# Performance work log

Hardware: AMD Instinct MI355X
Metric: run time of the kernel (lower is better)

Reference implementation:

```python
import jax, jax.numpy as jnp
import numpy as np

N_CLASSES = 16
REG = 0.1


def setup_inputs() -> dict:
    key = jax.random.key(0)
    k1, k2, k3, k4 = jax.random.split(key, 4)
    N, M, d = 4096, 4096, 1024
    X = jax.random.normal(k1, (N, d), dtype=jnp.float32)
    y = jax.random.randint(k2, (N,), 0, N_CLASSES)
    Xq = jax.random.normal(k3, (M, d), dtype=jnp.float32)
    m = 0.01 * jax.random.normal(k4, (1, d), dtype=jnp.float32)
    kappa = jnp.asarray(0.1, dtype=jnp.float32)
    nu = jnp.asarray(float(d), dtype=jnp.float32)
    triu_diag = jnp.ones((d,), dtype=jnp.float32)
    triu_lower = jnp.eye(d, dtype=jnp.float32) + 0.01 * jax.random.normal(
        jax.random.fold_in(key, 7), (d, d), dtype=jnp.float32)
    return {"X": X, "y": y, "Xq": Xq, "m": m, "kappa": kappa, "nu": nu,
            "triu_diag": triu_diag, "triu_lower": triu_lower}


def reference(X, y, Xq, m, kappa, nu, triu_diag, triu_lower):
    d = X.shape[1]
    C = N_CLASSES
    # Cholesky-factor prior scale: diag(|triu_diag|) + strictly-lower part of triu_lower
    strict_lower = jnp.tril(jnp.ones((d, d), dtype=X.dtype), -1)
    L = jnp.diag(jnp.abs(triu_diag)) + triu_lower * strict_lower
    kap = jnp.abs(kappa) + 1e-6
    nu_ = jnp.maximum(nu, d - 1 + 1e-6)

    # --- fit (vectorized over classes) ---
    onehot = jax.nn.one_hot(y, C, dtype=X.dtype)          # [N, C]
    Nj = onehot.sum(axis=0)                               # [C]
    sums = onehot.T @ X                                   # [C, d] grouped sums
    means = sums / Nj[:, None]                            # [C, d]
    mu = (kap / (kap + Nj))[:, None] * m + (Nj / (kap + Nj))[:, None] * means  # [C, d]
    # grouped scatter: S[c] = X_c^T X_c, via class-weighted features
    Xw = X[:, None, :] * onehot[:, :, None]               # [N, C, d]
    S = jnp.einsum('ncd,ne->cde', Xw, X)                  # [C, d, d]
    base = L @ L.T + kap * (m.T @ m)                      # [d, d]
    sigma = (base[None] + S
             - (kap + Nj)[:, None, None] * jnp.einsum('cd,ce->cde', mu, mu))
    sigma = sigma / (nu_ + Nj + d + 2)[:, None, None]     # [C, d, d]
    eye = jnp.eye(d, dtype=X.dtype)
    sigma_inv = (1.0 - REG) * jnp.linalg.inv(sigma) + REG * eye[None]

    # --- predict: negative Mahalanobis quadratic form per (query, class) ---
    diff = Xq[:, None, :] - mu[None]                      # [M, C, d]
    logits = -jnp.einsum('mcd,cde,mce->mc', diff, sigma_inv, diff)  # [M, C]
    return logits
```

## Files before the change

### kernel.cpp

```cpp
#include <hip/hip_runtime.h>
#include <math.h>

#define DD 1024
#define NP 5120
#define PT_TILES 80
#define TS 65

typedef _Float16 half8 __attribute__((ext_vector_type(8)));
typedef _Float16 half4 __attribute__((ext_vector_type(4)));
typedef float floatx4 __attribute__((ext_vector_type(4)));
typedef short s16x8 __attribute__((ext_vector_type(8)));

#define OFF_XTH   ((size_t)0)
#define OFF_XTL   ((size_t)2621440)
#define OFF_BASE  ((size_t)5242880)
#define OFF_SIGMA ((size_t)6291456)
#define OFF_DINV  ((size_t)23068672)
#define OFF_SUMS  ((size_t)24117248)
#define OFF_MU    ((size_t)24133632)
#define OFF_U     ((size_t)24150016)
#define OFF_MU2   ((size_t)24166400)
#define OFF_XQ2   ((size_t)24166416)
#define OFF_XQMU  ((size_t)24170512)
#define OFF_KAPNU ((size_t)24236048)
#define OFF_CF    ((size_t)24236056)
#define OFF_BETA  ((size_t)24236072)
#define OFF_INVS  ((size_t)24236088)
#define OFF_INTS  ((size_t)24236104)

#define UT_CLS_STRIDE ((size_t)557056)

__device__ __forceinline__ void tri_decode(int b, int& ti, int& tj) {
  int t = 0;
  while ((t + 1) * (t + 2) / 2 <= b) t++;
  ti = t;
  tj = b - t * (t + 1) / 2;
}

__device__ __forceinline__ short f2bf(float f) {
  union { float f; unsigned u; } v; v.f = f;
  unsigned r = v.u + 0x7FFF + ((v.u >> 16) & 1);
  return (short)(r >> 16);
}
__device__ __forceinline__ float bf2f(short b) {
  union { unsigned u; float f; } v; v.u = ((unsigned)(unsigned short)b) << 16; return v.f;
}

__device__ __forceinline__ float reduce256(float v, float* scratch) {
  for (int o = 32; o > 0; o >>= 1) v += __shfl_down(v, o, 64);
  int lane = threadIdx.x & 63, w = threadIdx.x >> 6;
  __syncthreads();
  if (lane == 0) scratch[w] = v;
  __syncthreads();
  return scratch[0] + scratch[1] + scratch[2] + scratch[3];
}

__global__ void k_scalars(const int* y, const float* kappa, const float* nu,
                          float* kapnu, float* cf, float* beta, float* invs,
                          int* counts, int* offsets, int* cls_of_pt, int* order,
                          float* sums, float* uarr, float* dout) {
  __shared__ int h[16];
  __shared__ int cur[16];
  int t = threadIdx.x;
  if (t < 16) h[t] = 0;
  __syncthreads();
  for (int n = t; n < 4096; n += 256) atomicAdd(&h[y[n]], 1);
  __syncthreads();
  if (t == 0) {
    float kap = fabsf(kappa[0]) + 1e-6f;
    float nu_ = fmaxf(nu[0], 1024.0f - 1.0f + 1e-6f);
    kapnu[0] = kap; kapnu[1] = nu_;
    int off = 0, tile = 0;
    for (int c = 0; c < 16; c++) {
      counts[c] = h[c]; offsets[c] = off; cur[c] = off;
      cf[c] = (float)h[c];
      beta[c] = kap + (float)h[c];
      invs[c] = 1.0f / (nu_ + (float)h[c] + 1024.0f + 2.0f);
      int ntile = ((h[c] + 63) & ~63) >> 6;
      for (int q = 0; q < ntile && tile < PT_TILES; q++) cls_of_pt[tile++] = c;
      off += (h[c] + 63) & ~63;
    }
    while (tile < PT_TILES) cls_of_pt[tile++] = -1;
  }
  for (int i = t; i < NP; i += 256) order[i] = -1;
  for (int i = t; i < 16 * 1024; i += 256) { sums[i] = 0.f; uarr[i] = 0.f; }
  for (int i = t; i < 4096 * 16; i += 256) dout[i] = 0.f;
  __syncthreads();
  for (int n = t; n < 4096; n += 256) {
    int c = y[n];
    int p = atomicAdd(&cur[c], 1);
    order[p] = n;
  }
}

__global__ void k_gatherT(const float* X, const int* order, const int* cls_of_pt,
                          short* XTh, short* XTl, float* sums) {
  int pt = blockIdx.x, dt = blockIdx.y, t = threadIdx.x;
  __shared__ float T[64 * TS];
  __shared__ float CS[4 * 64];
  __shared__ int src[64];
  if (t < 64) src[t] = order[pt * 64 + t];
  __syncthreads();
  for (int i = 0; i < 4; i++) {
    int idx4 = i * 256 + t;
    int r = idx4 >> 4, c4 = (idx4 & 15) << 2;
    int s = src[r];
    float4 v = (s >= 0) ? *(const float4*)&X[(size_t)s * DD + dt * 64 + c4]
                        : make_float4(0.f, 0.f, 0.f, 0.f);
    T[r * TS + c4] = v.x; T[r * TS + c4 + 1] = v.y;
    T[r * TS + c4 + 2] = v.z; T[r * TS + c4 + 3] = v.w;
  }
  __syncthreads();
  for (int i = 0; i < 16; i++) {
    int lin = i * 256 + t;
    int d = lin >> 6, p = lin & 63;
    float v = T[p * TS + d];
    short hi = f2bf(v);
    float lov = v - bf2f(hi);
    size_t addr = (size_t)(dt * 64 + d) * NP + pt * 64 + p;
    XTh[addr] = hi;
    XTl[addr] = f2bf(lov);
  }
  int cls = cls_of_pt[pt];
  if (cls < 0) return;
  int g = t >> 6, d = t & 63;
  float s = 0.f;
  for (int p = g * 16; p < g * 16 + 16; p++) s += T[p * TS + d];
  CS[g * 64 + d] = s;
  __syncthreads();
  if (g == 0)
    atomicAdd(&sums[(size_t)cls * DD + dt * 64 + d],
              CS[d] + CS[64 + d] + CS[128 + d] + CS[192 + d]);
}

__global__ void k_mumu2(const float* sums, const float* m, const float* kapnu,
                        const float* cf, float* mu, float* mu2) {
  __shared__ float scratch[4];
  int c = blockIdx.x, t = threadIdx.x;
  float kap = kapnu[0];
  float denom = 1.0f / (kap + cf[c]);
  float s2 = 0.f;
  for (int j = t; j < DD; j += 256) {
    float v = (kap * m[j] + sums[(size_t)c * DD + j]) * denom;
    mu[(size_t)c * DD + j] = v;
    s2 += v * v;
  }
  float tot = reduce256(s2, scratch);
  if (t == 0) mu2[c] = tot;
}

__device__ __forceinline__ float lval(const float* td, const float* tl, int i, int j) {
  if (i == j) return fabsf(td[i]);
  if (i > j) return tl[(size_t)i * DD + j];
  return 0.f;
}

__global__ void k_base(const float* td, const float* tl, const float* m,
                       const float* kapnu, float* base) {
  int ti, tj; tri_decode(blockIdx.x, ti, tj);
  __shared__ float Ta[16][65], Tb[16][65];
  int t = threadIdx.x, tx = t & 15, ty = t >> 4;
  int r0 = ty * 4, c0 = tx * 4;
  float acc[4][4] = {};
  int kmax = (tj + 1) * 64;
  for (int kk = 0; kk < kmax; kk += 16) {
    __syncthreads();
    for (int idx = t; idx < 64 * 16; idx += 256) {
      int r = idx >> 4, p = idx & 15;
      Ta[p][r] = lval(td, tl, ti * 64 + r, kk + p);
      Tb[p][r] = lval(td, tl, tj * 64 + r, kk + p);
    }
    __syncthreads();
#pragma unroll
    for (int p = 0; p < 16; p++) {
      float av[4], bv[4];
#pragma unroll
      for (int a = 0; a < 4; a++) av[a] = Ta[p][r0 + a];
#pragma unroll
      for (int b = 0; b < 4; b++) bv[b] = Tb[p][c0 + b];
#pragma unroll
      for (int a = 0; a < 4; a++)
#pragma unroll
        for (int b = 0; b < 4; b++) acc[a][b] += av[a] * bv[b];
    }
  }
  float kap = kapnu[0];
#pragma unroll
  for (int a = 0; a < 4; a++)
#pragma unroll
    for (int b = 0; b < 4; b++) {
      int gi = ti * 64 + r0 + a, gj = tj * 64 + c0 + b;
      base[(size_t)gi * DD + gj] = acc[a][b] + kap * m[gi] * m[gj];
    }
}

__global__ __launch_bounds__(256) void k_syrk_mfma(const short* XTh, const short* XTl,
                                                   const float* base, const float* mu,
                                                   const float* beta, const float* invs,
                                                   const int* counts, const int* offsets,
                                                   float* sigma) {
  int bb = blockIdx.x;
  int cls = bb / 36, tr = bb % 36;
  int ti, tj; tri_decode(tr, ti, tj);
  int cnt = counts[cls], off = offsets[cls];
  float* Sg = sigma + ((size_t)cls << 20);
  const float* muc = mu + (size_t)cls * DD;
  __shared__ short Ah[128 * 40], Al[128 * 40], Bh[128 * 40], Bl[128 * 40];
  int t = threadIdx.x;
  int wave = t >> 6, lane = t & 63;
  int wr = wave >> 1, wc = wave & 1;
  int quad = lane >> 4, l15 = lane & 15;
  int i0 = ti * 128, j0 = tj * 128;
  bool same = (ti == tj);
  floatx4 acc[4][4];
#pragma unroll
  for (int a = 0; a < 4; a++)
#pragma unroll
    for (int b = 0; b < 4; b++) acc[a][b] = (floatx4){0.f, 0.f, 0.f, 0.f};
  for (int nn = 0; nn < cnt; nn += 32) {
    __syncthreads();
#pragma unroll
    for (int r = 0; r < 2; r++) {
      int lin = r * 256 + t;
      int row = lin >> 2, kg = (lin & 3) << 3;
      size_t sA = (size_t)(i0 + row) * NP + off + nn + kg;
      *(s16x8*)&Ah[row * 40 + kg] = *(const s16x8*)&XTh[sA];
      *(s16x8*)&Al[row * 40 + kg] = *(const s16x8*)&XTl[sA];
      if (!same) {
        size_t sB = (size_t)(j0 + row) * NP + off + nn + kg;
        *(s16x8*)&Bh[row * 40 + kg] = *(const s16x8*)&XTh[sB];
        *(s16x8*)&Bl[row * 40 + kg] = *(const s16x8*)&XTl[sB];
      }
    }
    __syncthreads();
    const short* PBh = same ? Ah : Bh;
    const short* PBl = same ? Al : Bl;
    s16x8 ah[4], al[4], bh[4], bl[4];
#pragma unroll
    for (int f = 0; f < 4; f++) {
      ah[f] = *(const s16x8*)&Ah[(wr * 64 + f * 16 + l15) * 40 + quad * 8];
      al[f] = *(const s16x8*)&Al[(wr * 64 + f * 16 + l15) * 40 + quad * 8];
      bh[f] = *(const s16x8*)&PBh[(wc * 64 + f * 16 + l15) * 40 + quad * 8];
      bl[f] = *(const s16x8*)&PBl[(wc * 64 + f * 16 + l15) * 40 + quad * 8];
    }
#pragma unroll
    for (int fi = 0; fi < 4; fi++)
#pragma unroll
      for (int fj = 0; fj < 4; fj++) {
        acc[fi][fj] = __builtin_amdgcn_mfma_f32_16x16x32_bf16(ah[fi], bh[fj], acc[fi][fj], 0, 0, 0);
        acc[fi][fj] = __builtin_amdgcn_mfma_f32_16x16x32_bf16(ah[fi], bl[fj], acc[fi][fj], 0, 0, 0);
        acc[fi][fj] = __builtin_amdgcn_mfma_f32_16x16x32_bf16(al[fi], bh[fj], acc[fi][fj], 0, 0, 0);
      }
  }
  float bet = beta[cls], isc = invs[cls];
#pragma unroll
  for (int fi = 0; fi < 4; fi++)
#pragma unroll
    for (int fj = 0; fj < 4; fj++)
#pragma unroll
      for (int reg = 0; reg < 4; reg++) {
        int gi = i0 + wr * 64 + fi * 16 + quad * 4 + reg;
        int gj = j0 + wc * 64 + fj * 16 + l15;
        float v = acc[fi][fj][reg] + base[(size_t)gi * DD + gj] - bet * muc[gi] * muc[gj];
        Sg[(size_t)gi * DD + gj] = v * isc;
      }
}

__device__ void chol_inv_reg(float areg[4][4], float* Dinv, int cls, int k, int t,
                             float* Asc, float* Wsc, float* Tsc) {
  __shared__ float colbuf[2][64];
  __shared__ float sdiag[64];
  int tx = t & 15, ty = t >> 4;
  int r0 = ty * 4, c0 = tx * 4;
  for (int j = 0; j < 63; j++) {
    float* cb = colbuf[j & 1];
    if (tx == (j >> 2)) {
      int jj = j & 3;
      cb[r0 + 0] = areg[0][jj];
      cb[r0 + 1] = areg[1][jj];
      cb[r0 + 2] = areg[2][jj];
      cb[r0 + 3] = areg[3][jj];
    }
    __syncthreads();
    float rd = 1.0f / cb[j];
    float rv[4], cv[4];
#pragma unroll
    for (int i = 0; i < 4; i++) rv[i] = cb[r0 + i];
#pragma unroll
    for (int b = 0; b < 4; b++) cv[b] = cb[c0 + b];
#pragma unroll
    for (int i = 0; i < 4; i++)
#pragma unroll
      for (int b = 0; b < 4; b++)
        if (c0 + b > j && c0 + b <= r0 + i)
          areg[i][b] -= rv[i] * cv[b] * rd;
  }
  __syncthreads();
  if (tx == ty) {
#pragma unroll
    for (int i = 0; i < 4; i++) sdiag[r0 + i] = 1.0f / sqrtf(areg[i][i]);
  }
  __syncthreads();
  float sd[4];
#pragma unroll
  for (int b = 0; b < 4; b++) sd[b] = sdiag[c0 + b];
#pragma unroll
  for (int i = 0; i < 4; i++)
#pragma unroll
    for (int b = 0; b < 4; b++) {
      float lv = (r0 + i >= c0 + b) ? areg[i][b] * sd[b] : 0.f;
      Asc[(r0 + i) * TS + c0 + b] = lv;
      Wsc[(r0 + i) * TS + c0 + b] = 0.f;
    }
  __syncthreads();
  if (t < 16) {
    int c = t * 4;
    float l[4][4], w[4][4];
#pragma unroll
    for (int i = 0; i < 4; i++)
#pragma unroll
      for (int j = 0; j <= i; j++) l[i][j] = Asc[(c + i) * TS + c + j];
#pragma unroll
    for (int j = 0; j < 4; j++) {
      w[j][j] = 1.0f / l[j][j];
#pragma unroll
      for (int i = j + 1; i < 4; i++) {
        float s = 0.f;
#pragma unroll
        for (int kk = j; kk < i; kk++) s += l[i][kk] * w[kk][j];
        w[i][j] = -s / l[i][i];
      }
    }
#pragma unroll
    for (int i = 0; i < 4; i++)
#pragma unroll
      for (int j = 0; j <= i; j++) Wsc[(c + i) * TS + c + j] = w[i][j];
  }
  __syncthreads();
#pragma unroll 4
  for (int h = 4; h <= 32; h <<= 1) {
    int hh = h * h;
    int total = 32 * h;
    for (int idx = t; idx < total; idx += 256) {
      int pr = idx / hh;
      int rem = idx - pr * hh;
      int i = rem / h, j = rem - (rem / h) * h;
      int c = pr * 2 * h;
      float s = 0.f;
      for (int kk = j; kk < h; kk++)
        s += Asc[(c + h + i) * TS + c + kk] * Wsc[(c + kk) * TS + c + j];
      Tsc[idx] = s;
    }
    __syncthreads();
    for (int idx = t; idx < total; idx += 256) {
      int pr = idx / hh;
      int rem = idx - pr * hh;
      int i = rem / h, j = rem - (rem / h) * h;
      int c = pr * 2 * h;
      int tb = pr * hh;
      float s = 0.f;
      for (int kk = 0; kk <= i; kk++)
        s += Wsc[(c + h + i) * TS + c + h + kk] * Tsc[tb + kk * h + j];
      Wsc[(c + h + i) * TS + c + j] = -s;
    }
    __syncthreads();
  }
  float* Dv = Dinv + ((size_t)(cls * 16 + k)) * 4096;
  for (int idx4 = t; idx4 < 1024; idx4 += 256) {
    int r = idx4 >> 4, c4 = (idx4 & 15) << 2;
    float4 v = make_float4(Wsc[r * TS + c4], Wsc[r * TS + c4 + 1],
                           Wsc[r * TS + c4 + 2], Wsc[r * TS + c4 + 3]);
    *(float4*)&Dv[r * 64 + c4] = v;
  }
}

__global__ void k_diag0(float* sigma, float* Dinv) {
  __shared__ float A[64 * TS], W[64 * TS];
  __shared__ float Tq[1024];
  int cls = blockIdx.x, t = threadIdx.x;
  int tx = t & 15, ty = t >> 4;
  int r0 = ty * 4, c0 = tx * 4;
  float* Sg = sigma + ((size_t)cls << 20);
  float areg[4][4];
#pragma unroll
  for (int i = 0; i < 4; i++) {
    float4 s = *(const float4*)&Sg[(size_t)(r0 + i) * DD + c0];
    areg[i][0] = s.x; areg[i][1] = s.y; areg[i][2] = s.z; areg[i][3] = s.w;
  }
  chol_inv_reg(areg, Dinv, cls, 0, t, A, W, Tq);
}

__global__ void k_cholstep(float* sigma, float* Dinv, int k) {
  __shared__ float B0[64 * TS], B1[64 * TS], B2[64 * TS];
  int b = blockIdx.x, t = threadIdx.x;
  int tx = t & 15, ty = t >> 4;
  int r0 = ty * 4, c0 = tx * 4;
  int nb = 15 - k;
  int nt = nb * (nb + 1) / 2;
  int cls, a_, b_;
  bool special = (b < 16);
  if (special) { cls = b; a_ = 0; b_ = 0; }
  else {
    int jp = b - 16;
    cls = jp / (nt - 1);
    int s = jp % (nt - 1) + 1;
    tri_decode(s, a_, b_);
  }
  int it = k + 1 + a_, jt = k + 1 + b_;
  bool same = (it == jt);
  float* Sg = sigma + ((size_t)cls << 20);
  const float* Dv = Dinv + ((size_t)(cls * 16 + k)) * 4096;
  for (int i = 0; i < 4; i++) {
    int idx4 = i * 256 + t;
    int r = idx4 >> 4, c4 = (idx4 & 15) << 2;
    float4 v0 = *(const float4*)&Dv[r * 64 + c4];
    B0[r * TS + c4] = v0.x; B0[r * TS + c4 + 1] = v0.y;
    B0[r * TS + c4 + 2] = v0.z; B0[r * TS + c4 + 3] = v0.w;
    float4 v1 = *(const float4*)&Sg[(size_t)(it * 64 + r) * DD + k * 64 + c4];
    B1[r * TS + c4] = v1.x; B1[r * TS + c4 + 1] = v1.y;
    B1[r * TS + c4 + 2] = v1.z; B1[r * TS + c4 + 3] = v1.w;
    if (!same) {
      float4 v2 = *(const float4*)&Sg[(size_t)(jt * 64 + r) * DD + k * 64 + c4];
      B2[r * TS + c4] = v2.x; B2[r * TS + c4 + 1] = v2.y;
      B2[r * TS + c4 + 2] = v2.z; B2[r * TS + c4 + 3] = v2.w;
    }
  }
  __syncthreads();
  float a1[4][4] = {}, a2[4][4] = {};
#pragma unroll 8
  for (int p = 0; p < 64; p++) {
    float bv[4], av1[4];
#pragma unroll
    for (int bq = 0; bq < 4; bq++) bv[bq] = B0[(c0 + bq) * TS + p];
#pragma unroll
    for (int a = 0; a < 4; a++) av1[a] = B1[(r0 + a) * TS + p];
#pragma unroll
    for (int a = 0; a < 4; a++)
#pragma unroll
      for (int bq = 0; bq < 4; bq++) a1[a][bq] += av1[a] * bv[bq];
    if (!same) {
      float av2[4];
#pragma unroll
      for (int a = 0; a < 4; a++) av2[a] = B2[(r0 + a) * TS + p];
#pragma unroll
      for (int a = 0; a < 4; a++)
#pragma unroll
        for (int bq = 0; bq < 4; bq++) a2[a][bq] += av2[a] * bv[bq];
    }
  }
  __syncthreads();
#pragma unroll
  for (int a = 0; a < 4; a++)
#pragma unroll
    for (int bq = 0; bq < 4; bq++) {
      B1[(r0 + a) * TS + c0 + bq] = a1[a][bq];
      if (!same) B2[(r0 + a) * TS + c0 + bq] = a2[a][bq];
    }
  if (b_ == 0) {
#pragma unroll
    for (int a = 0; a < 4; a++) {
      float4 v = make_float4(a1[a][0], a1[a][1], a1[a][2], a1[a][3]);
      *(float4*)&Sg[(size_t)(k * 64 + r0 + a) * DD + it * 64 + c0] = v;
    }
  }
  __syncthreads();
  float* PB = same ? B1 : B2;
  float a3[4][4] = {};
#pragma unroll 8
  for (int p = 0; p < 64; p++) {
    float av[4], bv[4];
#pragma unroll
    for (int a = 0; a < 4; a++) av[a] = B1[(r0 + a) * TS + p];
#pragma unroll
    for (int bq = 0; bq < 4; bq++) bv[bq] = PB[(c0 + bq) * TS + p];
#pragma unroll
    for (int a = 0; a < 4; a++)
#pragma unroll
      for (int bq = 0; bq < 4; bq++) a3[a][bq] += av[a] * bv[bq];
  }
  if (!special) {
#pragma unroll
    for (int a = 0; a < 4; a++) {
      size_t addr = (size_t)(it * 64 + r0 + a) * DD + jt * 64 + c0;
      float4 s = *(const float4*)&Sg[addr];
      s.x -= a3[a][0]; s.y -= a3[a][1]; s.z -= a3[a][2]; s.w -= a3[a][3];
      *(float4*)&Sg[addr] = s;
    }
    return;
  }
  float areg[4][4];
#pragma unroll
  for (int i = 0; i < 4; i++) {
    size_t addr = (size_t)(it * 64 + r0 + i) * DD + jt * 64 + c0;
    float4 s = *(const float4*)&Sg[addr];
    areg[i][0] = s.x - a3[i][0]; areg[i][1] = s.y - a3[i][1];
    areg[i][2] = s.z - a3[i][2]; areg[i][3] = s.w - a3[i][3];
  }
  __syncthreads();
  chol_inv_reg(areg, Dinv, cls, k + 1, t, B1, B2, B0);
}

__global__ void k_vl1(float* sigma, const float* Dinv) {
  __shared__ float Rl[64 * TS], W0s[64 * TS], W1s[64 * TS], Ts[64 * TS];
  int b = blockIdx.x, t = threadIdx.x;
  int cls = b >> 3, i = b & 7;
  int t0 = 2 * i, t1 = 2 * i + 1;
  float* Sg = sigma + ((size_t)cls << 20);
  int tx = t & 15, ty = t >> 4;
  int r0 = ty * 4, c0 = tx * 4;
  const float* Dv0 = Dinv + ((size_t)(cls * 16 + t0)) * 4096;
  const float* Dv1 = Dinv + ((size_t)(cls * 16 + t1)) * 4096;
  for (int idx4 = t; idx4 < 1024; idx4 += 256) {
    int r = idx4 >> 4, c4 = (idx4 & 15) << 2;
    float4 vr = *(const float4*)&Sg[(size_t)(t0 * 64 + r) * DD + t1 * 64 + c4];
    Rl[r * TS + c4] = vr.x; Rl[r * TS + c4 + 1] = vr.y;
    Rl[r * TS + c4 + 2] = vr.z; Rl[r * TS + c4 + 3] = vr.w;
    float4 v0 = *(const float4*)&Dv0[r * 64 + c4];
    W0s[r * TS + c4] = v0.x; W0s[r * TS + c4 + 1] = v0.y;
    W0s[r * TS + c4 + 2] = v0.z; W0s[r * TS + c4 + 3] = v0.w;
    float4 v1 = *(const float4*)&Dv1[r * 64 + c4];
    W1s[r * TS + c4] = v1.x; W1s[r * TS + c4 + 1] = v1.y;
    W1s[r * TS + c4 + 2] = v1.z; W1s[r * TS + c4 + 3] = v1.w;
  }
  __syncthreads();
  float aT[4][4] = {};
#pragma unroll 8
  for (int p = 0; p < 64; p++) {
    float av[4], bv[4];
#pragma unroll
    for (int a = 0; a < 4; a++) av[a] = Rl[(r0 + a) * TS + p];
#pragma unroll
    for (int bq = 0; bq < 4; bq++) bv[bq] = W0s[p * TS + c0 + bq];
#pragma unroll
    for (int a = 0; a < 4; a++)
#pragma unroll
      for (int bq = 0; bq < 4; bq++) aT[a][bq] += av[a] * bv[bq];
  }
  __syncthreads();
#pragma unroll
  for (int a = 0; a < 4; a++)
#pragma unroll
    for (int bq = 0; bq < 4; bq++) Ts[(r0 + a) * TS + c0 + bq] = aT[a][bq];
  __syncthreads();
  float aV[4][4] = {};
#pragma unroll 8
  for (int p = 0; p < 64; p++) {
    float av[4], bv[4];
#pragma unroll
    for (int a = 0; a < 4; a++) av[a] = W1s[(r0 + a) * TS + p];
#pragma unroll
    for (int bq = 0; bq < 4; bq++) bv[bq] = Ts[p * TS + c0 + bq];
#pragma unroll
    for (int a = 0; a < 4; a++)
#pragma unroll
      for (int bq = 0; bq < 4; bq++) aV[a][bq] += av[a] * bv[bq];
  }
#pragma unroll
  for (int a = 0; a < 4; a++)
    *(float4*)&Sg[(size_t)(t0 * 64 + r0 + a) * DD + t1 * 64 + c0] =
        make_float4(-aV[a][0], -aV[a][1], -aV[a][2], -aV[a][3]);
}

__global__ void k_vlA(float* sigma, const float* Dinv, int w) {
  __shared__ float Xs[64 * TS], Ys[64 * TS];
  int aa = blockIdx.x / w, bb = blockIdx.x % w;
  int base = blockIdx.y * 2 * w, cls = blockIdx.z;
  float* Sg = sigma + ((size_t)cls << 20);
  int t = threadIdx.x, tx = t & 15, ty = t >> 4;
  int r0 = ty * 4, c0 = tx * 4;
  float acc[4][4] = {};
  for (int m = bb; m < w; m++) {
    __syncthreads();
    for (int idx4 = t; idx4 < 1024; idx4 += 256) {
      int r = idx4 >> 4, c4 = (idx4 & 15) << 2;
      float4 v = *(const float4*)&Sg[(size_t)((base + m) * 64 + r) * DD + (base + w + aa) * 64 + c4];
      Xs[r * TS + c4] = v.x; Xs[r * TS + c4 + 1] = v.y;
      Xs[r * TS + c4 + 2] = v.z; Xs[r * TS + c4 + 3] = v.w;
    }
    if (m == bb) {
      const float* Dv = Dinv + ((size_t)(cls * 16 + base + bb)) * 4096;
      for (int idx4 = t; idx4 < 1024; idx4 += 256) {
        int r = idx4 >> 4, c4 = (idx4 & 15) << 2;
        float4 v = *(const float4*)&Dv[r * 64 + c4];
        Ys[r * TS + c4] = v.x; Ys[r * TS + c4 + 1] = v.y;
        Ys[r * TS + c4 + 2] = v.z; Ys[r * TS + c4 + 3] = v.w;
      }
    } else {
      for (int idx4 = t; idx4 < 1024; idx4 += 256) {
        int p = idx4 >> 4, c4 = (idx4 & 15) << 2;
        float4 v = *(const float4*)&Sg[(size_t)((base + bb) * 64 + p) * DD + (base + m) * 64 + c4];
        Ys[p * TS + c4] = v.x; Ys[p * TS + c4 + 1] = v.y;
        Ys[p * TS + c4 + 2] = v.z; Ys[p * TS + c4 + 3] = v.w;
      }
    }
    __syncthreads();
#pragma unroll 8
    for (int p = 0; p < 64; p++) {
      float av[4], bv[4];
#pragma unroll
      for (int a = 0; a < 4; a++) av[a] = Xs[(r0 + a) * TS + p];
#pragma unroll
      for (int bq = 0; bq < 4; bq++) bv[bq] = Ys[p * TS + c0 + bq];
#pragma unroll
      for (int a = 0; a < 4; a++)
#pragma unroll
        for (int bq = 0; bq < 4; bq++) acc[a][bq] += av[a] * bv[bq];
    }
  }
#pragma unroll
  for (int a = 0; a < 4; a++)
    *(float4*)&Sg[(size_t)((base + w + aa) * 64 + r0 + a) * DD + (base + bb) * 64 + c0] =
        make_float4(acc[a][0], acc[a][1], acc[a][2], acc[a][3]);
}

__global__ void k_vlB(float* sigma, const float* Dinv, int w) {
  __shared__ float Xs[64 * TS], Ys[64 * TS];
  int aa = blockIdx.x / w, bb = blockIdx.x % w;
  int base = blockIdx.y * 2 * w, cls = blockIdx.z;
  float* Sg = sigma + ((size_t)cls << 20);
  int t = threadIdx.x, tx = t & 15, ty = t >> 4;
  int r0 = ty * 4, c0 = tx * 4;
  float acc[4][4] = {};
  for (int m = 0; m <= aa; m++) {
    __syncthreads();
    if (m == aa) {
      const float* Dv = Dinv + ((size_t)(cls * 16 + base + w + aa)) * 4096;
      for (int idx4 = t; idx4 < 1024; idx4 += 256) {
        int r = idx4 >> 4, c4 = (idx4 & 15) << 2;
        float4 v = *(const float4*)&Dv[r * 64 + c4];
        Xs[r * TS + c4] = v.x; Xs[r * TS + c4 + 1] = v.y;
        Xs[r * TS + c4 + 2] = v.z; Xs[r * TS + c4 + 3] = v.w;
      }
    } else {
      for (int idx4 = t; idx4 < 1024; idx4 += 256) {
        int r = idx4 >> 4, c4 = (idx4 & 15) << 2;
        float4 v = *(const float4*)&Sg[(size_t)((base + w + m) * 64 + r) * DD + (base + w + aa) * 64 + c4];
        Xs[r * TS + c4] = v.x; Xs[r * TS + c4 + 1] = v.y;
        Xs[r * TS + c4 + 2] = v.z; Xs[r * TS + c4 + 3] = v.w;
      }
    }
    for (int idx4 = t; idx4 < 1024; idx4 += 256) {
      int p = idx4 >> 4, c4 = (idx4 & 15) << 2;
      float4 v = *(const float4*)&Sg[(size_t)((base + w + m) * 64 + p) * DD + (base + bb) * 64 + c4];
      Ys[p * TS + c4] = v.x; Ys[p * TS + c4 + 1] = v.y;
      Ys[p * TS + c4 + 2] = v.z; Ys[p * TS + c4 + 3] = v.w;
    }
    __syncthreads();
#pragma unroll 8
    for (int p = 0; p < 64; p++) {
      float av[4], bv[4];
#pragma unroll
      for (int a = 0; a < 4; a++) av[a] = Xs[(r0 + a) * TS + p];
#pragma unroll
      for (int bq = 0; bq < 4; bq++) bv[bq] = Ys[p * TS + c0 + bq];
#pragma unroll
      for (int a = 0; a < 4; a++)
#pragma unroll
        for (int bq = 0; bq < 4; bq++) acc[a][bq] += av[a] * bv[bq];
    }
  }
#pragma unroll
  for (int a = 0; a < 4; a++)
    *(float4*)&Sg[(size_t)((base + bb) * 64 + r0 + a) * DD + (base + w + aa) * 64 + c0] =
        make_float4(-acc[a][0], -acc[a][1], -acc[a][2], -acc[a][3]);
}

__global__ void k_finalize(const float* sigma, const float* Dinv, const float* mu,
                           float* uarr, _Float16* UT) {
  __shared__ float U0[64 * TS];
  __shared__ float CS[4 * 64];
  int jp = blockIdx.x, t = threadIdx.x;
  int cls = jp / 136, tr = jp % 136;
  int nt_, kt_; tri_decode(tr, nt_, kt_);
  const float* muc = mu + (size_t)cls * DD;
  _Float16* outp = UT + (size_t)cls * UT_CLS_STRIDE + (size_t)tr * 4096;
  const float* srcp;
  size_t row_stride;
  if (kt_ == nt_) {
    srcp = Dinv + ((size_t)(cls * 16 + nt_)) * 4096;
    row_stride = 64;
  } else {
    srcp = sigma + ((size_t)cls << 20) + (size_t)(kt_ * 64) * DD + nt_ * 64;
    row_stride = DD;
  }
  for (int i = 0; i < 2; i++) {
    int g8 = i * 256 + t;
    int rr = g8 >> 3, c8 = (g8 & 7) << 3;
    float4 v0 = *(const float4*)&srcp[(size_t)rr * row_stride + c8];
    float4 v1 = *(const float4*)&srcp[(size_t)rr * row_stride + c8 + 4];
    half8 h;
    h[0] = (_Float16)v0.x; h[1] = (_Float16)v0.y; h[2] = (_Float16)v0.z; h[3] = (_Float16)v0.w;
    h[4] = (_Float16)v1.x; h[5] = (_Float16)v1.y; h[6] = (_Float16)v1.z; h[7] = (_Float16)v1.w;
    *(half8*)&outp[rr * 64 + c8] = h;
    U0[rr * TS + c8] = v0.x; U0[rr * TS + c8 + 1] = v0.y;
    U0[rr * TS + c8 + 2] = v0.z; U0[rr * TS + c8 + 3] = v0.w;
    U0[rr * TS + c8 + 4] = v1.x; U0[rr * TS + c8 + 5] = v1.y;
    U0[rr * TS + c8 + 6] = v1.z; U0[rr * TS + c8 + 7] = v1.w;
  }
  __syncthreads();
  int g = t >> 6, r = t & 63;
  float s = 0.f;
  for (int c = g * 16; c < g * 16 + 16; c++)
    s += U0[r * TS + c] * muc[kt_ * 64 + c];
  CS[g * 64 + r] = s;
  __syncthreads();
  if (g == 0)
    atomicAdd(&uarr[(size_t)cls * DD + nt_ * 64 + r],
              CS[r] + CS[64 + r] + CS[128 + r] + CS[192 + r]);
}

__global__ void k_xqdots(const float* Xq, const float* mu, float* xq2, float* xqmu,
                         _Float16* XqH) {
  __shared__ float xrow[DD];
  int m = blockIdx.x, t = threadIdx.x;
  for (int i = t; i < 256; i += 256)
    ((float4*)xrow)[i] = ((const float4*)(Xq + (size_t)m * DD))[i];
  __syncthreads();
  for (int i = t; i < 256; i += 256) {
    float4 v = ((const float4*)xrow)[i];
    half4 h = {(_Float16)v.x, (_Float16)v.y, (_Float16)v.z, (_Float16)v.w};
    *(half4*)&XqH[(size_t)m * DD + i * 4] = h;
  }
  int wave = t >> 6, lane = t & 63;
  for (int cc = 0; cc < 4; cc++) {
    int c = wave * 4 + cc;
    const float* muc = mu + (size_t)c * DD;
    float s = 0.f;
    for (int j = lane; j < DD; j += 64) s += xrow[j] * muc[j];
    for (int o = 32; o > 0; o >>= 1) s += __shfl_down(s, o, 64);
    if (lane == 0) xqmu[(size_t)m * 16 + c] = s;
  }
  if (wave == 0) {
    float s = 0.f;
    for (int j = lane; j < DD; j += 64) s += xrow[j] * xrow[j];
    for (int o = 32; o > 0; o >>= 1) s += __shfl_down(s, o, 64);
    if (lane == 0) xq2[m] = s;
  }
}

__global__ __launch_bounds__(256) void k_gemmG_mfma(const _Float16* XqH, const _Float16* UT,
                                                    const float* u, float* dout) {
  int mt = blockIdx.x, ct = blockIdx.y, cls = blockIdx.z;
  const _Float16* Uc = UT + (size_t)cls * UT_CLS_STRIDE;
  __shared__ _Float16 As[128 * 40];
  __shared__ _Float16 Bs[128 * 40];
  int t = threadIdx.x;
  int wave = t >> 6, lane = t & 63;
  int wr = wave >> 1, wc = wave & 1;
  int quad = lane >> 4, l15 = lane & 15;
  int m0 = mt * 128, n0 = ct * 128, NT0 = ct * 2;
  floatx4 acc[4][4];
#pragma unroll
  for (int a = 0; a < 4; a++)
#pragma unroll
    for (int b = 0; b < 4; b++) acc[a][b] = (floatx4){0.f, 0.f, 0.f, 0.f};
  int kmax = (ct + 1) * 128;
  for (int kk = 0; kk < kmax; kk += 32) {
    __syncthreads();
#pragma unroll
    for (int i = 0; i < 2; i++) {
      int lin = i * 256 + t;
      int r = lin >> 2, kg = (lin & 3) * 8;
      *(half8*)&As[r * 40 + kg] = *(const half8*)&XqH[(size_t)(m0 + r) * DD + kk + kg];
    }
    int kt = kk >> 6, k0 = kk & 63;
#pragma unroll
    for (int i = 0; i < 2; i++) {
      int lin = i * 256 + t;
      int nl = lin >> 2, kg = (lin & 3) * 8;
      int s = nl >> 6, np = nl & 63;
      int nt = NT0 + s;
      half8 v = {};
      if (kt <= nt)
        v = *(const half8*)&Uc[(size_t)(nt * (nt + 1) / 2 + kt) * 4096 + np * 64 + k0 + kg];
      *(half8*)&Bs[nl * 40 + kg] = v;
    }
    __syncthreads();
    half8 af[4], bf[4];
#pragma unroll
    for (int f = 0; f < 4; f++) {
      af[f] = *(const half8*)&As[(wr * 64 + f * 16 + l15) * 40 + quad * 8];
      bf[f] = *(const half8*)&Bs[(wc * 64 + f * 16 + l15) * 40 + quad * 8];
    }
#pragma unroll
    for (int fi = 0; fi < 4; fi++)
#pragma unroll
      for (int fj = 0; fj < 4; fj++)
        acc[fi][fj] = __builtin_amdgcn_mfma_f32_16x16x32_f16(af[fi], bf[fj], acc[fi][fj], 0, 0, 0);
  }
  float uv[4];
#pragma unroll
  for (int fj = 0; fj < 4; fj++)
    uv[fj] = u[(size_t)cls * DD + n0 + wc * 64 + fj * 16 + l15];
#pragma unroll
  for (int fi = 0; fi < 4; fi++) {
#pragma unroll
    for (int r = 0; r < 4; r++) {
      float p = 0.f;
#pragma unroll
      for (int fj = 0; fj < 4; fj++) {
        float e = acc[fi][fj][r] - uv[fj];
        p += e * e;
      }
      p += __shfl_xor(p, 1, 64);
      p += __shfl_xor(p, 2, 64);
      p += __shfl_xor(p, 4, 64);
      p += __shfl_xor(p, 8, 64);
      if (l15 == 0) {
        int m = m0 + wr * 64 + fi * 16 + quad * 4 + r;
        atomicAdd(&dout[(size_t)m * 16 + cls], p);
      }
    }
  }
}

__global__ void k_logits(const float* xq2, const float* xqmu, const float* mu2,
                         float* dout) {
  size_t idx = (size_t)blockIdx.x * 256 + threadIdx.x;
  int m = (int)(idx >> 4), c = (int)(idx & 15);
  float q1 = dout[idx];
  float q2 = xq2[m] - 2.0f * xqmu[idx] + mu2[c];
  dout[idx] = -(0.9f * q1 + 0.1f * q2);
}

extern "C" void kernel_launch(void* const* d_in, const int* in_sizes, int n_in,
                              void* d_out, int out_size, void* d_ws, size_t ws_size,
                              hipStream_t stream) {
  (void)in_sizes; (void)n_in; (void)out_size; (void)ws_size;
  const float* X  = (const float*)d_in[0];
  const int*   y  = (const int*)d_in[1];
  const float* Xq = (const float*)d_in[2];
  const float* m  = (const float*)d_in[3];
  const float* kappa = (const float*)d_in[4];
  const float* nu = (const float*)d_in[5];
  const float* td = (const float*)d_in[6];
  const float* tl = (const float*)d_in[7];
  float* out = (float*)d_out;
  float* ws = (float*)d_ws;

  short* XTh   = (short*)(ws + OFF_XTH);
  short* XTl   = (short*)(ws + OFF_XTL);
  _Float16* UT = (_Float16*)ws;
  float* baseb = ws + OFF_BASE;
  float* sigma = ws + OFF_SIGMA;
  _Float16* XqH = (_Float16*)sigma;
  float* Dinv  = ws + OFF_DINV;
  float* sums  = ws + OFF_SUMS;
  float* mu    = ws + OFF_MU;
  float* uarr  = ws + OFF_U;
  float* mu2   = ws + OFF_MU2;
  float* xq2   = ws + OFF_XQ2;
  float* xqmu  = ws + OFF_XQMU;
  float* kapnu = ws + OFF_KAPNU;
  float* cf    = ws + OFF_CF;
  float* beta  = ws + OFF_BETA;
  float* invs  = ws + OFF_INVS;
  int* ints      = (int*)(ws + OFF_INTS);
  int* counts    = ints;
  int* offsets   = ints + 16;
  int* cls_of_pt = ints + 32;
  int* order     = ints + 32 + PT_TILES;

  k_scalars<<<1, 256, 0, stream>>>(y, kappa, nu, kapnu, cf, beta, invs,
                                   counts, offsets, cls_of_pt, order,
                                   sums, uarr, out);
  k_gatherT<<<dim3(PT_TILES, 16), 256, 0, stream>>>(X, order, cls_of_pt, XTh, XTl, sums);
  k_mumu2<<<16, 256, 0, stream>>>(sums, m, kapnu, cf, mu, mu2);
  k_base<<<136, 256, 0, stream>>>(td, tl, m, kapnu, baseb);
  k_syrk_mfma<<<16 * 36, 256, 0, stream>>>(XTh, XTl, baseb, mu, beta, invs,
                                           counts, offsets, sigma);
  k_diag0<<<16, 256, 0, stream>>>(sigma, Dinv);
  for (int k = 0; k < 15; k++) {
    int nb = 15 - k;
    int nt = nb * (nb + 1) / 2;
    k_cholstep<<<16 * nt, 256, 0, stream>>>(sigma, Dinv, k);
  }
  k_vl1<<<128, 256, 0, stream>>>(sigma, Dinv);
  for (int L = 2; L <= 4; L++) {
    int w = 1 << (L - 1);
    int ncomb = 8 >> (L - 1);
    k_vlA<<<dim3(w * w, ncomb, 16), 256, 0, stream>>>(sigma, Dinv, w);
    k_vlB<<<dim3(w * w, ncomb, 16), 256, 0, stream>>>(sigma, Dinv, w);
  }
  k_finalize<<<16 * 136, 256, 0, stream>>>(sigma, Dinv, mu, uarr, UT);
  k_xqdots<<<4096, 256, 0, stream>>>(Xq, mu, xq2, xqmu, XqH);
  k_gemmG_mfma<<<dim3(32, 8, 16), 256, 0, stream>>>(XqH, UT, uarr, out);
  k_logits<<<256, 256, 0, stream>>>(xq2, xqmu, mu2, out);
}
```

Before: 1.518 ms.

## Block the in-register 64x64 Cholesky into 8-column panels

```diff
diff --git a/kernel.cpp b/kernel.cpp
--- a/kernel.cpp
+++ b/kernel.cpp
@@ -268,47 +268,106 @@
 
 __device__ void chol_inv_reg(float areg[4][4], float* Dinv, int cls, int k, int t,
                              float* Asc, float* Wsc, float* Tsc) {
-  __shared__ float colbuf[2][64];
-  __shared__ float sdiag[64];
+  __shared__ float Pn[64 * 9];
   int tx = t & 15, ty = t >> 4;
   int r0 = ty * 4, c0 = tx * 4;
-  for (int j = 0; j < 63; j++) {
-    float* cb = colbuf[j & 1];
-    if (tx == (j >> 2)) {
-      int jj = j & 3;
-      cb[r0 + 0] = areg[0][jj];
-      cb[r0 + 1] = areg[1][jj];
-      cb[r0 + 2] = areg[2][jj];
-      cb[r0 + 3] = areg[3][jj];
-    }
-    __syncthreads();
-    float rd = 1.0f / cb[j];
-    float rv[4], cv[4];
-#pragma unroll
-    for (int i = 0; i < 4; i++) rv[i] = cb[r0 + i];
-#pragma unroll
-    for (int b = 0; b < 4; b++) cv[b] = cb[c0 + b];
-#pragma unroll
-    for (int i = 0; i < 4; i++)
-#pragma unroll
-      for (int b = 0; b < 4; b++)
-        if (c0 + b > j && c0 + b <= r0 + i)
-          areg[i][b] -= rv[i] * cv[b] * rd;
-  }
-  __syncthreads();
-  if (tx == ty) {
-#pragma unroll
-    for (int i = 0; i < 4; i++) sdiag[r0 + i] = 1.0f / sqrtf(areg[i][i]);
-  }
-  __syncthreads();
-  float sd[4];
-#pragma unroll
-  for (int b = 0; b < 4; b++) sd[b] = sdiag[c0 + b];
+  for (int jb = 0; jb < 8; jb++) {
+    int cb = jb * 8;
+    bool owner = ((tx >> 1) == jb);
+    if (owner && r0 + 3 >= cb) {
+#pragma unroll
+      for (int i = 0; i < 4; i++)
+        if (r0 + i >= cb) {
+#pragma unroll
+          for (int b = 0; b < 4; b++)
+            Pn[(r0 + i) * 9 + (c0 - cb) + b] = areg[i][b];
+        }
+    }
+    __syncthreads();
+    bool needR = (r0 >= cb + 8);
+    bool needC = (c0 >= cb + 8);
+    bool diagOwn = owner && ((ty >> 1) == jb);
+    bool setPanel = owner && needR;
+    bool doUpd = needR && needC;
+    if (setPanel || doUpd || diagOwn) {
+      float Ld[8][8], invd[8];
+#pragma unroll
+      for (int j = 0; j < 8; j++) {
+        float s = Pn[(cb + j) * 9 + j];
+#pragma unroll
+        for (int m = 0; m < 8; m++)
+          if (m < j) s -= Ld[j][m] * Ld[j][m];
+        float dv = sqrtf(s);
+        Ld[j][j] = dv;
+        invd[j] = 1.0f / dv;
+#pragma unroll
+        for (int i2 = 0; i2 < 8; i2++)
+          if (i2 > j) {
+            float v = Pn[(cb + i2) * 9 + j];
+#pragma unroll
+            for (int m = 0; m < 8; m++)
+              if (m < j) v -= Ld[i2][m] * Ld[j][m];
+            Ld[i2][j] = v * invd[j];
+          }
+      }
+      float Wr[4][8], Wc[4][8];
+      if (setPanel || doUpd) {
+#pragma unroll
+        for (int i = 0; i < 4; i++)
+#pragma unroll
+          for (int kq = 0; kq < 8; kq++) {
+            float v = Pn[(r0 + i) * 9 + kq];
+#pragma unroll
+            for (int m = 0; m < 8; m++)
+              if (m < kq) v -= Ld[kq][m] * Wr[i][m];
+            Wr[i][kq] = v * invd[kq];
+          }
+      }
+      if (doUpd) {
+#pragma unroll
+        for (int b = 0; b < 4; b++)
+#pragma unroll
+          for (int kq = 0; kq < 8; kq++) {
+            float v = Pn[(c0 + b) * 9 + kq];
+#pragma unroll
+            for (int m = 0; m < 8; m++)
+              if (m < kq) v -= Ld[kq][m] * Wc[b][m];
+            Wc[b][kq] = v * invd[kq];
+          }
+      }
+      if (diagOwn) {
+        int ro = r0 - cb, co = c0 - cb;
+#pragma unroll
+        for (int i = 0; i < 4; i++)
+#pragma unroll
+          for (int b = 0; b < 4; b++)
+            areg[i][b] = (ro + i >= co + b) ? Ld[ro + i][co + b] : 0.f;
+      } else if (setPanel) {
+        int co = c0 - cb;
+#pragma unroll
+        for (int i = 0; i < 4; i++)
+#pragma unroll
+          for (int b = 0; b < 4; b++)
+            areg[i][b] = Wr[i][co + b];
+      } else if (doUpd) {
+#pragma unroll
+        for (int i = 0; i < 4; i++)
+#pragma unroll
+          for (int b = 0; b < 4; b++) {
+            float s = 0.f;
+#pragma unroll
+            for (int m = 0; m < 8; m++) s += Wr[i][m] * Wc[b][m];
+            areg[i][b] -= s;
+          }
+      }
+    }
+    __syncthreads();
+  }
 #pragma unroll
   for (int i = 0; i < 4; i++)
 #pragma unroll
     for (int b = 0; b < 4; b++) {
-      float lv = (r0 + i >= c0 + b) ? areg[i][b] * sd[b] : 0.f;
+      float lv = (r0 + i >= c0 + b) ? areg[i][b] : 0.f;
       Asc[(r0 + i) * TS + c0 + b] = lv;
       Wsc[(r0 + i) * TS + c0 + b] = 0.f;
     }
```

New measurement: 1.931 ms. 1.27x slower.

## Split early Cholesky steps into panel solve and trailing update kernels

Applied to the files above, without the earlier changes.

```diff
diff --git a/kernel.cpp b/kernel.cpp
--- a/kernel.cpp
+++ b/kernel.cpp
@@ -388,6 +388,113 @@
     areg[i][0] = s.x; areg[i][1] = s.y; areg[i][2] = s.z; areg[i][3] = s.w;
   }
   chol_inv_reg(areg, Dinv, cls, 0, t, A, W, Tq);
+}
+
+__global__ void k_panel(float* sigma, const float* Dinv, int k) {
+  __shared__ float B0[64 * TS], B1[64 * TS];
+  int i_ = blockIdx.x, cls = blockIdx.y, t = threadIdx.x;
+  int tx = t & 15, ty = t >> 4;
+  int r0 = ty * 4, c0 = tx * 4;
+  int it = k + 1 + i_;
+  float* Sg = sigma + ((size_t)cls << 20);
+  const float* Dv = Dinv + ((size_t)(cls * 16 + k)) * 4096;
+  for (int i = 0; i < 4; i++) {
+    int idx4 = i * 256 + t;
+    int r = idx4 >> 4, c4 = (idx4 & 15) << 2;
+    float4 v0 = *(const float4*)&Dv[r * 64 + c4];
+    B0[r * TS + c4] = v0.x; B0[r * TS + c4 + 1] = v0.y;
+    B0[r * TS + c4 + 2] = v0.z; B0[r * TS + c4 + 3] = v0.w;
+    float4 v1 = *(const float4*)&Sg[(size_t)(it * 64 + r) * DD + k * 64 + c4];
+    B1[r * TS + c4] = v1.x; B1[r * TS + c4 + 1] = v1.y;
+    B1[r * TS + c4 + 2] = v1.z; B1[r * TS + c4 + 3] = v1.w;
+  }
+  __syncthreads();
+  float a1[4][4] = {};
+#pragma unroll 8
+  for (int p = 0; p < 64; p++) {
+    float bv[4], av1[4];
+#pragma unroll
+    for (int bq = 0; bq < 4; bq++) bv[bq] = B0[(c0 + bq) * TS + p];
+#pragma unroll
+    for (int a = 0; a < 4; a++) av1[a] = B1[(r0 + a) * TS + p];
+#pragma unroll
+    for (int a = 0; a < 4; a++)
+#pragma unroll
+      for (int bq = 0; bq < 4; bq++) a1[a][bq] += av1[a] * bv[bq];
+  }
+#pragma unroll
+  for (int a = 0; a < 4; a++) {
+    float4 v = make_float4(a1[a][0], a1[a][1], a1[a][2], a1[a][3]);
+    *(float4*)&Sg[(size_t)(k * 64 + r0 + a) * DD + it * 64 + c0] = v;
+  }
+}
+
+__global__ void k_update(float* sigma, float* Dinv, int k) {
+  __shared__ float B0[64 * TS], B1[64 * TS], B2[64 * TS];
+  int b = blockIdx.x, t = threadIdx.x;
+  int tx = t & 15, ty = t >> 4;
+  int r0 = ty * 4, c0 = tx * 4;
+  int nb = 15 - k;
+  int nt = nb * (nb + 1) / 2;
+  int cls, a_, b_;
+  bool special = (b < 16);
+  if (special) { cls = b; a_ = 0; b_ = 0; }
+  else {
+    int jp = b - 16;
+    cls = jp / (nt - 1);
+    int s = jp % (nt - 1) + 1;
+    tri_decode(s, a_, b_);
+  }
+  int it = k + 1 + a_, jt = k + 1 + b_;
+  bool same = (it == jt);
+  float* Sg = sigma + ((size_t)cls << 20);
+  for (int i = 0; i < 4; i++) {
+    int idx4 = i * 256 + t;
+    int r = idx4 >> 4, c4 = (idx4 & 15) << 2;
+    float4 v1 = *(const float4*)&Sg[(size_t)(k * 64 + r) * DD + it * 64 + c4];
+    B1[r * TS + c4] = v1.x; B1[r * TS + c4 + 1] = v1.y;
+    B1[r * TS + c4 + 2] = v1.z; B1[r * TS + c4 + 3] = v1.w;
+    if (!same) {
+      float4 v2 = *(const float4*)&Sg[(size_t)(k * 64 + r) * DD + jt * 64 + c4];
+      B2[r * TS + c4] = v2.x; B2[r * TS + c4 + 1] = v2.y;
+      B2[r * TS + c4 + 2] = v2.z; B2[r * TS + c4 + 3] = v2.w;
+    }
+  }
+  __syncthreads();
+  float* PB = same ? B1 : B2;
+  float a3[4][4] = {};
+#pragma unroll 8
+  for (int p = 0; p < 64; p++) {
+    float av[4], bv[4];
+#pragma unroll
+    for (int a = 0; a < 4; a++) av[a] = B1[(r0 + a) * TS + p];
+#pragma unroll
+    for (int bq = 0; bq < 4; bq++) bv[bq] = PB[(c0 + bq) * TS + p];
+#pragma unroll
+    for (int a = 0; a < 4; a++)
+#pragma unroll
+      for (int bq = 0; bq < 4; bq++) a3[a][bq] += av[a] * bv[bq];
+  }
+  if (!special) {
+#pragma unroll
+    for (int a = 0; a < 4; a++) {
+      size_t addr = (size_t)(it * 64 + r0 + a) * DD + jt * 64 + c0;
+      float4 s = *(const float4*)&Sg[addr];
+      s.x -= a3[a][0]; s.y -= a3[a][1]; s.z -= a3[a][2]; s.w -= a3[a][3];
+      *(float4*)&Sg[addr] = s;
+    }
+    return;
+  }
+  float areg[4][4];
+#pragma unroll
+  for (int i = 0; i < 4; i++) {
+    size_t addr = (size_t)(it * 64 + r0 + i) * DD + jt * 64 + c0;
+    float4 s = *(const float4*)&Sg[addr];
+    areg[i][0] = s.x - a3[i][0]; areg[i][1] = s.y - a3[i][1];
+    areg[i][2] = s.z - a3[i][2]; areg[i][3] = s.w - a3[i][3];
+  }
+  __syncthreads();
+  chol_inv_reg(areg, Dinv, cls, k + 1, t, B1, B2, B0);
 }
 
 __global__ void k_cholstep(float* sigma, float* Dinv, int k) {
@@ -873,7 +980,12 @@
   for (int k = 0; k < 15; k++) {
     int nb = 15 - k;
     int nt = nb * (nb + 1) / 2;
-    k_cholstep<<<16 * nt, 256, 0, stream>>>(sigma, Dinv, k);
+    if (k <= 7) {
+      k_panel<<<dim3(nb, 16), 256, 0, stream>>>(sigma, Dinv, k);
+      k_update<<<16 * nt, 256, 0, stream>>>(sigma, Dinv, k);
+    } else {
+      k_cholstep<<<16 * nt, 256, 0, stream>>>(sigma, Dinv, k);
+    }
   }
   k_vl1<<<128, 256, 0, stream>>>(sigma, Dinv);
   for (int L = 2; L <= 4; L++) {
```

Result: faster. 1.488 ms (-2.0%).
